# Optimization experiments

Hardware: AMD Instinct MI355X
Metric: run time of the kernel (lower is better)

## Reference

```python
import jax, jax.numpy as jnp
import numpy as np

B, F = 4096, 16384          # batch, total features
G, S = 512, 32              # n_groups, group_size (F = G*S, contiguous partition)
UNITS = 1


def setup_inputs() -> dict:
    key = jax.random.key(0)
    k_x, k_w = jax.random.split(key)
    x = jax.random.normal(k_x, (B, F), dtype=jnp.float32)
    # contiguous non-overlapping groups: group g owns columns [g*S, (g+1)*S)
    group_idx = jnp.arange(G * S, dtype=jnp.int64).reshape(G, S)
    # per-group multiplicative-factor weights (GroupConnected.w, HeNormal ~ scaled normal)
    w_group = jax.random.normal(k_w, (G, S), dtype=jnp.float32) * jnp.sqrt(2.0 / S)
    # final Dense kernel, kernel_initializer=Ones in the original
    fc_kernel = jnp.ones((G, UNITS), dtype=jnp.float32)
    return {"x": x, "group_idx": group_idx, "w_group": w_group, "fc_kernel": fc_kernel}


def reference(x, group_idx, w_group, fc_kernel):
    # GroupConnected: per-group gather + weighted sum, vectorized as one gather + einsum.
    gathered = x[:, group_idx]                      # [B, G, S]
    gc = jnp.einsum('bgs,gs->bg', gathered, w_group)  # [B, G]
    # TibGroupLasso.fc: Dense(units, no bias)
    return gc @ fc_kernel                           # [B, units]
```

## Files before the change

### kernel.cpp

```cpp
#include <hip/hip_runtime.h>

#define BB 4096
#define FF 16384
#define GG 512
#define SS 32

typedef float v4f __attribute__((ext_vector_type(4)));

__global__ void build_v_kernel(const int* __restrict__ idx,
                               const float* __restrict__ w,
                               const float* __restrict__ fc,
                               float* __restrict__ v) {
    int i = blockIdx.x * blockDim.x + threadIdx.x;
    if (i < GG * SS) {
        int g = i >> 5;
        atomicAdd(&v[idx[i]], w[i] * fc[g]);
    }
}

__global__ __launch_bounds__(256) void gemv_kernel(const float* __restrict__ x,
                                                   const float* __restrict__ v,
                                                   float* __restrict__ out) {
    const int b = blockIdx.x;
    const v4f* __restrict__ x4 = (const v4f*)(x + (size_t)b * FF);
    const v4f* __restrict__ v4 = (const v4f*)v;

    v4f acc = {0.0f, 0.0f, 0.0f, 0.0f};
    #pragma unroll 8
    for (int i = threadIdx.x; i < FF / 4; i += 256) {
        v4f xv = __builtin_nontemporal_load(&x4[i]);
        v4f vv = v4[i];
        acc += xv * vv;
    }
    float sum = (acc.x + acc.y) + (acc.z + acc.w);

    #pragma unroll
    for (int off = 32; off > 0; off >>= 1)
        sum += __shfl_down(sum, off, 64);

    __shared__ float wsum[4];
    const int wave = threadIdx.x >> 6;
    if ((threadIdx.x & 63) == 0) wsum[wave] = sum;
    __syncthreads();
    if (threadIdx.x == 0)
        out[b] = wsum[0] + wsum[1] + wsum[2] + wsum[3];
}

extern "C" void kernel_launch(void* const* d_in, const int* in_sizes, int n_in,
                              void* d_out, int out_size, void* d_ws, size_t ws_size,
                              hipStream_t stream) {
    const float* x   = (const float*)d_in[0];
    const int*   idx = (const int*)d_in[1];
    const float* w   = (const float*)d_in[2];
    const float* fc  = (const float*)d_in[3];
    float* out = (float*)d_out;
    float* v   = (float*)d_ws;

    hipMemsetAsync(v, 0, FF * sizeof(float), stream);
    build_v_kernel<<<(GG * SS + 255) / 256, 256, 0, stream>>>(idx, w, fc, v);
    gemv_kernel<<<BB, 256, 0, stream>>>(x, v, out);
}
```

Baseline: 339.3 us.

## Map one row per wave in GEMV and drop memset and atomics in vector build

The GEMV kernel now assigns each wavefront its own batch row, with two independent accumulators and two loads per iteration. This removes the cross-wave shared-memory reduction and block barrier. The folded weight vector is now built with plain stores instead of zero-fill plus atomics, which removes the memset launch. That is only correct when every feature index appears exactly once in group_idx.

```diff
diff --git a/kernel.cpp b/kernel.cpp
--- a/kernel.cpp
+++ b/kernel.cpp
@@ -13,37 +13,37 @@
                                float* __restrict__ v) {
     int i = blockIdx.x * blockDim.x + threadIdx.x;
     if (i < GG * SS) {
-        int g = i >> 5;
-        atomicAdd(&v[idx[i]], w[i] * fc[g]);
+        v[idx[i]] = w[i] * fc[i >> 5];
     }
 }
 
 __global__ __launch_bounds__(256) void gemv_kernel(const float* __restrict__ x,
                                                    const float* __restrict__ v,
                                                    float* __restrict__ out) {
-    const int b = blockIdx.x;
-    const v4f* __restrict__ x4 = (const v4f*)(x + (size_t)b * FF);
+    const int wave = threadIdx.x >> 6;
+    const int lane = threadIdx.x & 63;
+    const int row  = (blockIdx.x << 2) + wave;
+
+    const v4f* __restrict__ x4 = (const v4f*)(x + (size_t)row * FF);
     const v4f* __restrict__ v4 = (const v4f*)v;
 
-    v4f acc = {0.0f, 0.0f, 0.0f, 0.0f};
-    #pragma unroll 8
-    for (int i = threadIdx.x; i < FF / 4; i += 256) {
-        v4f xv = __builtin_nontemporal_load(&x4[i]);
-        v4f vv = v4[i];
-        acc += xv * vv;
+    v4f acc0 = {0.0f, 0.0f, 0.0f, 0.0f};
+    v4f acc1 = {0.0f, 0.0f, 0.0f, 0.0f};
+    #pragma unroll 4
+    for (int i = lane; i < FF / 4; i += 128) {
+        v4f xa = __builtin_nontemporal_load(&x4[i]);
+        v4f xb = __builtin_nontemporal_load(&x4[i + 64]);
+        acc0 += xa * v4[i];
+        acc1 += xb * v4[i + 64];
     }
+    v4f acc = acc0 + acc1;
     float sum = (acc.x + acc.y) + (acc.z + acc.w);
 
     #pragma unroll
     for (int off = 32; off > 0; off >>= 1)
         sum += __shfl_down(sum, off, 64);
 
-    __shared__ float wsum[4];
-    const int wave = threadIdx.x >> 6;
-    if ((threadIdx.x & 63) == 0) wsum[wave] = sum;
-    __syncthreads();
-    if (threadIdx.x == 0)
-        out[b] = wsum[0] + wsum[1] + wsum[2] + wsum[3];
+    if (lane == 0) out[row] = sum;
 }
 
 extern "C" void kernel_launch(void* const* d_in, const int* in_sizes, int n_in,
@@ -56,7 +56,6 @@
     float* out = (float*)d_out;
     float* v   = (float*)d_ws;
 
-    hipMemsetAsync(v, 0, FF * sizeof(float), stream);
     build_v_kernel<<<(GG * SS + 255) / 256, 256, 0, stream>>>(idx, w, fc, v);
-    gemv_kernel<<<BB, 256, 0, stream>>>(x, v, out);
+    gemv_kernel<<<BB / 4, 256, 0, stream>>>(x, v, out);
 }
```

Measured after the change: 338.1 us. No clear change (-0.4%).
